# Kernel tuning notes

Measured on AMD Instinct MI355X. Metric: run time of the kernel, lower is better.

## Reference

```python
import jax, jax.numpy as jnp
import numpy as np

IN_DIM = 1024
OUT_DIM = 1024
NUM_HEADS = 16
DEPTH = IN_DIM // NUM_HEADS  # 64


def setup_inputs() -> dict:
    key = jax.random.key(0)
    ks = jax.random.split(key, 11)
    B, S = 8, 1024  # S must equal IN_DIM (reshape constraint in original module)
    s_in = 1.0 / np.sqrt(IN_DIM)
    return {
        "query": jax.random.normal(ks[0], (B, S, IN_DIM), jnp.float32),
        "key": jax.random.normal(ks[1], (B, S, IN_DIM), jnp.float32),
        "value": jax.random.normal(ks[2], (B, S, IN_DIM), jnp.float32),
        "Wq": jax.random.normal(ks[3], (IN_DIM, IN_DIM), jnp.float32) * s_in,
        "bq": jnp.zeros((IN_DIM,), jnp.float32),
        "Wk": jax.random.normal(ks[4], (IN_DIM, IN_DIM), jnp.float32) * s_in,
        "bk": jnp.zeros((IN_DIM,), jnp.float32),
        "Wv": jax.random.normal(ks[5], (IN_DIM, IN_DIM), jnp.float32) * s_in,
        "bv": jnp.zeros((IN_DIM,), jnp.float32),
        "Wo": jax.random.normal(ks[6], (OUT_DIM, IN_DIM), jnp.float32) * s_in,
        "bo": jnp.zeros((OUT_DIM,), jnp.float32),
    }


def reference(query, key, value, Wq, bq, Wk, bk, Wv, bv, Wo, bo):
    B, S, D = query.shape
    H, P = NUM_HEADS, DEPTH

    def split_heads(x):
        # (B,S,D) -> (B,S,H,P) -> transpose last two dims -> (B,S,P,H)
        return x.reshape(B, S, H, P).swapaxes(-1, -2)

    Q = split_heads(query @ Wq.T + bq)   # (B,S,P,H)
    K = split_heads(key @ Wk.T + bk)     # (B,S,P,H)
    V = split_heads(value @ Wv.T + bv)   # (B,S,P,H)

    scale = jnp.sqrt(jnp.float32(P))
    # scores over the depth axis, per (batch, token): (B,S,P,P)
    scores = jnp.einsum('bsph,bsqh->bspq', Q, K) / scale
    # original uses softmax over dim=0 (the batch axis) - reproduce faithfully
    attn = jax.nn.softmax(scores, axis=0)
    out = jnp.einsum('bspq,bsqh->bsph', attn, V)   # (B,S,P,H)
    # transpose(-1,-2) -> (B,S,H,P), reshape to (B,S,S) (requires H*P == S)
    out = out.swapaxes(-1, -2).reshape(B, S, S)
    out = out @ Wo.T + bo                           # (B,S,OUT_DIM)
    return jax.nn.sigmoid(out)
```

## Files before the change

### kernel.cpp

```cpp
#include <hip/hip_runtime.h>


using short8  = __attribute__((ext_vector_type(8))) short;
using floatx4 = __attribute__((ext_vector_type(4))) float;

__device__ __forceinline__ float bf2f(unsigned short u) {
    return __uint_as_float(((unsigned)u) << 16);
}
__device__ __forceinline__ unsigned short f2bf(float f) {
    unsigned u = __float_as_uint(f);
    u += 0x7fffu + ((u >> 16) & 1u);
    return (unsigned short)(u >> 16);
}
__device__ __forceinline__ unsigned pack_trunc(float f0, float f1) {
    return __builtin_amdgcn_perm(__float_as_uint(f1), __float_as_uint(f0), 0x07060302u);
}
__device__ __forceinline__ void async_ld16(const void* g, void* l) {
    __builtin_amdgcn_global_load_lds(
        (const __attribute__((address_space(1))) unsigned int*)g,
        (__attribute__((address_space(3))) unsigned int*)l, 16, 0, 0);
}

__device__ __forceinline__ void conv8(const float* src, unsigned short* d, size_t i) {
    float4 a = *(const float4*)(src + i);
    float4 b = *(const float4*)(src + i + 4);
    uint4 o;
    o.x = ((unsigned)f2bf(a.y) << 16) | f2bf(a.x);
    o.y = ((unsigned)f2bf(a.w) << 16) | f2bf(a.z);
    o.z = ((unsigned)f2bf(b.y) << 16) | f2bf(b.x);
    o.w = ((unsigned)f2bf(b.w) << 16) | f2bf(b.z);
    *(uint4*)(d + i) = o;
}

__global__ __launch_bounds__(256) void convert_weights(
    const float* __restrict__ w0, const float* __restrict__ w1,
    const float* __restrict__ w2, const float* __restrict__ w3,
    unsigned short* __restrict__ dst)
{
    const float* srcs[4] = {w0, w1, w2, w3};
    conv8(srcs[blockIdx.y], dst + (size_t)blockIdx.y * (1024u * 1024u),
          ((size_t)blockIdx.x * 256 + threadIdx.x) * 8);
}

__global__ __launch_bounds__(256) void convert_acts(
    const float* __restrict__ a0, const float* __restrict__ a1,
    const float* __restrict__ a2, unsigned short* __restrict__ dst)
{
    const float* srcs[3] = {a0, a1, a2};
    conv8(srcs[blockIdx.y], dst + (size_t)blockIdx.y * ((size_t)8192 * 1024),
          ((size_t)blockIdx.x * 256 + threadIdx.x) * 8);
}

template<bool AF32, bool SIG>
__global__ __launch_bounds__(256) void gemm128(
    const void* __restrict__ A0, const void* __restrict__ A1, const void* __restrict__ A2,
    const unsigned short* __restrict__ W0, const unsigned short* __restrict__ W1,
    const unsigned short* __restrict__ W2,
    const float* __restrict__ b0, const float* __restrict__ b1, const float* __restrict__ b2,
    void* __restrict__ C0, void* __restrict__ C1, void* __restrict__ C2)
{
    const int z = blockIdx.z;
    const void* Ap = (z == 0) ? A0 : (z == 1) ? A1 : A2;
    const unsigned short* W = (z == 0) ? W0 : (z == 1) ? W1 : W2;
    const float* bias = (z == 0) ? b0 : (z == 1) ? b1 : b2;
    void* Cp = (z == 0) ? C0 : (z == 1) ? C1 : C2;

    constexpr int Kd = 1024, Nd = 1024;
    const int t = threadIdx.x;
    const int w = t >> 6, lane = t & 63;
    const int l15 = lane & 15, quad = lane >> 4;
    const int blockM = blockIdx.x * 128;
    const int blockN = blockIdx.y * 128;
    const int wy = w >> 1, wx = w & 1;

    __shared__ unsigned short Bs[128 * 32];
    constexpr int ABYTES = AF32 ? (128 * 32 * 4) : (128 * 32 * 2);
    __shared__ __align__(16) unsigned char AsRaw[ABYTES];
    float* AsF = (float*)AsRaw;
    unsigned short* AsB = (unsigned short*)AsRaw;

    const int br  = lane >> 2;
    const int bg  = (lane & 3) ^ (br & 3);
    const unsigned short* Bsrc0 = W + (size_t)(blockN + w * 32 + br) * Kd + bg * 8;
    const unsigned short* Bsrc1 = Bsrc0 + (size_t)16 * Kd;
    unsigned short* Bdst0 = &Bs[(w * 2 + 0) * 512];
    unsigned short* Bdst1 = &Bs[(w * 2 + 1) * 512];

    const int ar = lane >> 3;
    const int ag = (lane & 7) ^ (ar & 7);
    const float* AsrcF[4];
    float* AdstF[4];
    const unsigned short* AsrcB0 = nullptr; const unsigned short* AsrcB1 = nullptr;
    unsigned short* AdstB0 = nullptr; unsigned short* AdstB1 = nullptr;
    if (AF32) {
        #pragma unroll
        for (int j = 0; j < 4; ++j) {
            AsrcF[j] = (const float*)Ap + (size_t)(blockM + w * 32 + j * 8 + ar) * Kd + ag * 4;
            AdstF[j] = AsF + (w * 4 + j) * 256;
        }
    } else {
        AsrcB0 = (const unsigned short*)Ap + (size_t)(blockM + w * 32 + br) * Kd + bg * 8;
        AsrcB1 = AsrcB0 + (size_t)16 * Kd;
        AdstB0 = &AsB[(w * 2 + 0) * 512];
        AdstB1 = &AsB[(w * 2 + 1) * 512];
    }

    floatx4 acc[4][4] = {};

    for (int k0 = 0; k0 < Kd; k0 += 32) {
        if (AF32) {
            #pragma unroll
            for (int j = 0; j < 4; ++j) async_ld16(AsrcF[j] + k0, AdstF[j]);
        } else {
            async_ld16(AsrcB0 + k0, AdstB0);
            async_ld16(AsrcB1 + k0, AdstB1);
        }
        async_ld16(Bsrc0 + k0, Bdst0);
        async_ld16(Bsrc1 + k0, Bdst1);
        __syncthreads();

        short8 af[4], bfr[4];
        #pragma unroll
        for (int mt = 0; mt < 4; ++mt) {
            const int row = wy * 64 + mt * 16 + l15;
            if (AF32) {
                const int r7 = l15 & 7;
                const float* ap = AsF + row * 32;
                float4 lo = *(const float4*)(ap + (((quad * 2 + 0) ^ r7) * 4));
                float4 hi = *(const float4*)(ap + (((quad * 2 + 1) ^ r7) * 4));
                union { unsigned u[4]; short8 s; } cv;
                cv.u[0] = pack_trunc(lo.x, lo.y);
                cv.u[1] = pack_trunc(lo.z, lo.w);
                cv.u[2] = pack_trunc(hi.x, hi.y);
                cv.u[3] = pack_trunc(hi.z, hi.w);
                af[mt] = cv.s;
            } else {
                af[mt] = *(const short8*)&AsB[row * 32 + (quad ^ (l15 & 3)) * 8];
            }
        }
        #pragma unroll
        for (int nt = 0; nt < 4; ++nt) {
            const int row = wx * 64 + nt * 16 + l15;
            bfr[nt] = *(const short8*)&Bs[row * 32 + (quad ^ (l15 & 3)) * 8];
        }
        #pragma unroll
        for (int mt = 0; mt < 4; ++mt)
            #pragma unroll
            for (int nt = 0; nt < 4; ++nt)
                acc[mt][nt] = __builtin_amdgcn_mfma_f32_16x16x32_bf16(af[mt], bfr[nt], acc[mt][nt], 0, 0, 0);
        __syncthreads();
    }

    #pragma unroll
    for (int nt = 0; nt < 4; ++nt) {
        const int col = blockN + wx * 64 + nt * 16 + l15;
        const float bv = bias[col];
        #pragma unroll
        for (int mt = 0; mt < 4; ++mt) {
            const int row = blockM + wy * 64 + mt * 16 + quad * 4;
            #pragma unroll
            for (int r = 0; r < 4; ++r) {
                float v = acc[mt][nt][r] + bv;
                if (SIG) {
                    v = 1.0f / (1.0f + __expf(-v));
                    ((float*)Cp)[(size_t)(row + r) * Nd + col] = v;
                } else {
                    ((unsigned short*)Cp)[(size_t)(row + r) * Nd + col] = f2bf(v);
                }
            }
        }
    }
}

__device__ __forceinline__ float dot4q(const float* qf, ushort4 k) {
    return qf[0] * bf2f(k.x) + qf[1] * bf2f(k.y) + qf[2] * bf2f(k.z) + qf[3] * bf2f(k.w);
}
__device__ __forceinline__ void axpy4(float* o, float w, ushort4 v) {
    o[0] += w * bf2f(v.x); o[1] += w * bf2f(v.y); o[2] += w * bf2f(v.z); o[3] += w * bf2f(v.w);
}

__global__ __launch_bounds__(512) void attn_kernel(
    const unsigned short* __restrict__ Q,
    const unsigned short* __restrict__ Kt,
    const unsigned short* __restrict__ Vt,
    unsigned short* __restrict__ O2)
{
    constexpr int QS = 20;
    constexpr int PB = 64 * QS + 4;
    __shared__ unsigned short Kl[8 * PB];
    __shared__ unsigned short Vl[8 * PB];
    __shared__ unsigned short Ql[8 * PB];

    const int s = blockIdx.x;
    const int t = threadIdx.x;
    const int b8 = t >> 6, lq = t & 63;

    {
        const size_t gbase = ((size_t)b8 * 1024 + s) * 1024;
        const unsigned short* Ks = Kt + gbase;
        const unsigned short* Vs = Vt + gbase;
        const unsigned short* Qs = Q  + gbase;
        unsigned* kd = (unsigned*)&Kl[b8 * PB + lq * QS];
        unsigned* vd = (unsigned*)&Vl[b8 * PB + lq * QS];
        unsigned* qd = (unsigned*)&Ql[b8 * PB + lq * QS];
        #pragma unroll
        for (int w2 = 0; w2 < 8; ++w2) {
            unsigned klo = Ks[(2 * w2) * 64 + lq], khi = Ks[(2 * w2 + 1) * 64 + lq];
            kd[w2] = klo | (khi << 16);
            unsigned vlo = Vs[(2 * w2) * 64 + lq], vhi = Vs[(2 * w2 + 1) * 64 + lq];
            vd[w2] = vlo | (vhi << 16);
            unsigned qlo = Qs[(2 * w2) * 64 + lq], qhi = Qs[(2 * w2 + 1) * 64 + lq];
            qd[w2] = qlo | (qhi << 16);
        }
    }
    __syncthreads();

    const int b = t & 7;
    const int p = t >> 3;

    float qf[16], o[16];
    {
        const unsigned short* qp = &Ql[b * PB + p * QS];
        #pragma unroll
        for (int h4 = 0; h4 < 4; ++h4) {
            ushort4 qv = *(const ushort4*)&qp[h4 * 4];
            qf[h4 * 4 + 0] = bf2f(qv.x); qf[h4 * 4 + 1] = bf2f(qv.y);
            qf[h4 * 4 + 2] = bf2f(qv.z); qf[h4 * 4 + 3] = bf2f(qv.w);
        }
        #pragma unroll
        for (int h = 0; h < 16; ++h) o[h] = 0.0f;
    }

    const unsigned short* kp = &Kl[b * PB];
    const unsigned short* vp = &Vl[b * PB];

    for (int q = 0; q < 64; ++q) {
        const int off = q * QS;
        float sc = dot4q(qf + 0,  *(const ushort4*)&kp[off + 0])
                 + dot4q(qf + 4,  *(const ushort4*)&kp[off + 4])
                 + dot4q(qf + 8,  *(const ushort4*)&kp[off + 8])
                 + dot4q(qf + 12, *(const ushort4*)&kp[off + 12]);
        float e = __expf(sc * 0.125f);
        float d = e;
        d += __shfl_xor(d, 1);
        d += __shfl_xor(d, 2);
        d += __shfl_xor(d, 4);
        const float wgt = e * __builtin_amdgcn_rcpf(d);
        axpy4(o + 0,  wgt, *(const ushort4*)&vp[off + 0]);
        axpy4(o + 4,  wgt, *(const ushort4*)&vp[off + 4]);
        axpy4(o + 8,  wgt, *(const ushort4*)&vp[off + 8]);
        axpy4(o + 12, wgt, *(const ushort4*)&vp[off + 12]);
    }

    {
        unsigned* od = (unsigned*)&Ql[b * PB + p * QS];
        #pragma unroll
        for (int w2 = 0; w2 < 8; ++w2)
            od[w2] = ((unsigned)f2bf(o[2 * w2 + 1]) << 16) | f2bf(o[2 * w2]);
    }
    __syncthreads();

    {
        const size_t gbase = ((size_t)b8 * 1024 + s) * 1024;
        const unsigned* qd = (const unsigned*)&Ql[b8 * PB + lq * QS];
        #pragma unroll
        for (int w2 = 0; w2 < 8; ++w2) {
            unsigned v = qd[w2];
            O2[gbase + (2 * w2) * 64 + lq]     = (unsigned short)(v & 0xffff);
            O2[gbase + (2 * w2 + 1) * 64 + lq] = (unsigned short)(v >> 16);
        }
    }
}

extern "C" void kernel_launch(void* const* d_in, const int* in_sizes, int n_in,
                              void* d_out, int out_size, void* d_ws, size_t ws_size,
                              hipStream_t stream) {
    const float* query = (const float*)d_in[0];
    const float* key_  = (const float*)d_in[1];
    const float* value = (const float*)d_in[2];
    const float* Wq = (const float*)d_in[3];
    const float* bq = (const float*)d_in[4];
    const float* Wk = (const float*)d_in[5];
    const float* bk = (const float*)d_in[6];
    const float* Wv = (const float*)d_in[7];
    const float* bv = (const float*)d_in[8];
    const float* Wo = (const float*)d_in[9];
    const float* bo = (const float*)d_in[10];

    const size_t WN = (size_t)1024 * 1024;
    const size_t MN = (size_t)8192 * 1024;

    unsigned short* Wbf = (unsigned short*)d_ws;
    unsigned short* Wq_bf = Wbf;
    unsigned short* Wk_bf = Wbf + WN;
    unsigned short* Wv_bf = Wbf + 2 * WN;
    unsigned short* Wo_bf = Wbf + 3 * WN;

    convert_weights<<<dim3(512, 4), dim3(256), 0, stream>>>(Wq, Wk, Wv, Wo, Wbf);

    const bool big = ws_size >= (4 * WN + 6 * MN) * sizeof(unsigned short);

    unsigned short* Qb; unsigned short* Kb; unsigned short* Vb;
    if (big) {
        unsigned short* abf = Wbf + 4 * WN;
        Qb = abf + 3 * MN; Kb = Qb + MN; Vb = Kb + MN;
        convert_acts<<<dim3(4096, 3), dim3(256), 0, stream>>>(query, key_, value, abf);
        gemm128<false, false><<<dim3(64, 8, 3), dim3(256), 0, stream>>>(
            abf, abf + MN, abf + 2 * MN, Wq_bf, Wk_bf, Wv_bf, bq, bk, bv, Qb, Kb, Vb);
    } else {
        Qb = Wbf + 4 * WN; Kb = Qb + MN; Vb = Kb + MN;
        gemm128<true, false><<<dim3(64, 8, 3), dim3(256), 0, stream>>>(
            query, key_, value, Wq_bf, Wk_bf, Wv_bf, bq, bk, bv, Qb, Kb, Vb);
    }

    unsigned short* O2 = Qb;
    attn_kernel<<<dim3(1024), dim3(512), 0, stream>>>(Qb, Kb, Vb, O2);

    gemm128<false, true><<<dim3(64, 8, 1), dim3(256), 0, stream>>>(
        O2, O2, O2, Wo_bf, Wo_bf, Wo_bf, bo, bo, bo, d_out, d_out, d_out);
}
```

Baseline: 329.0 us.

## Rewrite batch-axis attention with MFMA score and PV products

Replaces the scalar per-thread dot-product attention kernel with one that computes QK^T and attn·V through bf16 MFMA instructions. The batch-axis softmax is done as a separate pass over exp scores staged in LDS. The grid is split in two along the query-row dimension, so each block handles 32 rows of P. This trades scalar FMA work for matrix-core throughput, at the cost of extra LDS staging and syncs, bf16 truncation of the exp values, and K/V being loaded twice across the two halves. Because O2 aliases Q, correctness depends on each half writing only its own 32-row slice.

```diff
diff --git a/kernel.cpp b/kernel.cpp
--- a/kernel.cpp
+++ b/kernel.cpp
@@ -1,8 +1,9 @@
 #include <hip/hip_runtime.h>
 
 
-using short8  = __attribute__((ext_vector_type(8))) short;
-using floatx4 = __attribute__((ext_vector_type(4))) float;
+using short8   = __attribute__((ext_vector_type(8))) short;
+using floatx4  = __attribute__((ext_vector_type(4))) float;
+using floatx16 = __attribute__((ext_vector_type(16))) float;
 
 __device__ __forceinline__ float bf2f(unsigned short u) {
     return __uint_as_float(((unsigned)u) << 16);
@@ -172,102 +173,140 @@
     }
 }
 
-__device__ __forceinline__ float dot4q(const float* qf, ushort4 k) {
-    return qf[0] * bf2f(k.x) + qf[1] * bf2f(k.y) + qf[2] * bf2f(k.z) + qf[3] * bf2f(k.w);
-}
-__device__ __forceinline__ void axpy4(float* o, float w, ushort4 v) {
-    o[0] += w * bf2f(v.x); o[1] += w * bf2f(v.y); o[2] += w * bf2f(v.z); o[3] += w * bf2f(v.w);
-}
-
-__global__ __launch_bounds__(512) void attn_kernel(
+__global__ __launch_bounds__(512) void attn_mfma(
     const unsigned short* __restrict__ Q,
     const unsigned short* __restrict__ Kt,
     const unsigned short* __restrict__ Vt,
     unsigned short* __restrict__ O2)
 {
-    constexpr int QS = 20;
-    constexpr int PB = 64 * QS + 4;
-    __shared__ unsigned short Kl[8 * PB];
-    __shared__ unsigned short Vl[8 * PB];
-    __shared__ unsigned short Ql[8 * PB];
-
-    const int s = blockIdx.x;
-    const int t = threadIdx.x;
-    const int b8 = t >> 6, lq = t & 63;
-
-    {
-        const size_t gbase = ((size_t)b8 * 1024 + s) * 1024;
-        const unsigned short* Ks = Kt + gbase;
-        const unsigned short* Vs = Vt + gbase;
-        const unsigned short* Qs = Q  + gbase;
-        unsigned* kd = (unsigned*)&Kl[b8 * PB + lq * QS];
-        unsigned* vd = (unsigned*)&Vl[b8 * PB + lq * QS];
-        unsigned* qd = (unsigned*)&Ql[b8 * PB + lq * QS];
-        #pragma unroll
-        for (int w2 = 0; w2 < 8; ++w2) {
-            unsigned klo = Ks[(2 * w2) * 64 + lq], khi = Ks[(2 * w2 + 1) * 64 + lq];
-            kd[w2] = klo | (khi << 16);
-            unsigned vlo = Vs[(2 * w2) * 64 + lq], vhi = Vs[(2 * w2 + 1) * 64 + lq];
-            vd[w2] = vlo | (vhi << 16);
-            unsigned qlo = Qs[(2 * w2) * 64 + lq], qhi = Qs[(2 * w2 + 1) * 64 + lq];
-            qd[w2] = qlo | (qhi << 16);
-        }
-    }
-    __syncthreads();
-
-    const int b = t & 7;
-    const int p = t >> 3;
-
-    float qf[16], o[16];
-    {
-        const unsigned short* qp = &Ql[b * PB + p * QS];
-        #pragma unroll
-        for (int h4 = 0; h4 < 4; ++h4) {
-            ushort4 qv = *(const ushort4*)&qp[h4 * 4];
-            qf[h4 * 4 + 0] = bf2f(qv.x); qf[h4 * 4 + 1] = bf2f(qv.y);
-            qf[h4 * 4 + 2] = bf2f(qv.z); qf[h4 * 4 + 3] = bf2f(qv.w);
-        }
-        #pragma unroll
-        for (int h = 0; h < 16; ++h) o[h] = 0.0f;
-    }
-
-    const unsigned short* kp = &Kl[b * PB];
-    const unsigned short* vp = &Vl[b * PB];
-
-    for (int q = 0; q < 64; ++q) {
-        const int off = q * QS;
-        float sc = dot4q(qf + 0,  *(const ushort4*)&kp[off + 0])
-                 + dot4q(qf + 4,  *(const ushort4*)&kp[off + 4])
-                 + dot4q(qf + 8,  *(const ushort4*)&kp[off + 8])
-                 + dot4q(qf + 12, *(const ushort4*)&kp[off + 12]);
-        float e = __expf(sc * 0.125f);
-        float d = e;
-        d += __shfl_xor(d, 1);
-        d += __shfl_xor(d, 2);
-        d += __shfl_xor(d, 4);
-        const float wgt = e * __builtin_amdgcn_rcpf(d);
-        axpy4(o + 0,  wgt, *(const ushort4*)&vp[off + 0]);
-        axpy4(o + 4,  wgt, *(const ushort4*)&vp[off + 4]);
-        axpy4(o + 8,  wgt, *(const ushort4*)&vp[off + 8]);
-        axpy4(o + 12, wgt, *(const ushort4*)&vp[off + 12]);
-    }
-
-    {
-        unsigned* od = (unsigned*)&Ql[b * PB + p * QS];
-        #pragma unroll
-        for (int w2 = 0; w2 < 8; ++w2)
-            od[w2] = ((unsigned)f2bf(o[2 * w2 + 1]) << 16) | f2bf(o[2 * w2]);
-    }
-    __syncthreads();
-
-    {
-        const size_t gbase = ((size_t)b8 * 1024 + s) * 1024;
-        const unsigned* qd = (const unsigned*)&Ql[b8 * PB + lq * QS];
-        #pragma unroll
-        for (int w2 = 0; w2 < 8; ++w2) {
-            unsigned v = qd[w2];
-            O2[gbase + (2 * w2) * 64 + lq]     = (unsigned short)(v & 0xffff);
-            O2[gbase + (2 * w2 + 1) * 64 + lq] = (unsigned short)(v >> 16);
+    constexpr int VOFF = 0;
+    constexpr int UOFF = 9216;
+    constexpr int QOFF = UOFF + 8192;
+    __shared__ __align__(16) unsigned short lds[UOFF + 18432];
+
+    const int s  = blockIdx.x;
+    const int ph = blockIdx.y;
+    const int t  = threadIdx.x;
+    const int w  = t >> 6;
+    const int l  = t & 63;
+    const int l15 = l & 15, l31 = l & 31, half = l >> 5, quad = l >> 4;
+
+    const size_t gb = ((size_t)w * 1024 + s) * 1024;
+
+    {
+        const unsigned* vg = (const unsigned*)(Vt + gb);
+        unsigned* vd = (unsigned*)lds;
+        #pragma unroll
+        for (int it = 0; it < 8; ++it) {
+            const int h = it * 2 + half;
+            vd[w * 576 + h * 36 + l31] = vg[h * 32 + l31];
+        }
+        const unsigned short* kg = Kt + gb;
+        unsigned* kd = (unsigned*)(lds + UOFF);
+        #pragma unroll
+        for (int h2 = 0; h2 < 8; ++h2) {
+            unsigned klo = kg[(2 * h2) * 64 + l];
+            unsigned khi = kg[(2 * h2 + 1) * 64 + l];
+            kd[w * 512 + l * 8 + h2] = klo | (khi << 16);
+        }
+        const unsigned short* qg = Q + gb + ph * 32;
+        unsigned* qd = (unsigned*)(lds + QOFF);
+        #pragma unroll
+        for (int it = 0; it < 4; ++it) {
+            const int h = it * 4 + half * 2;
+            unsigned qlo = qg[h * 64 + l31];
+            unsigned qhi = qg[(h + 1) * 64 + l31];
+            qd[w * 256 + l31 * 8 + it * 2 + half] = qlo | (qhi << 16);
+        }
+    }
+    __syncthreads();
+
+    floatx16 sc[2];
+    {
+        short8 qf = *(const short8*)&lds[QOFF + w * 512 + l31 * 16 + half * 8];
+        short8 kf0 = *(const short8*)&lds[UOFF + w * 1024 + l31 * 16 + half * 8];
+        short8 kf1 = *(const short8*)&lds[UOFF + w * 1024 + (32 + l31) * 16 + half * 8];
+        floatx16 z = {};
+        sc[0] = __builtin_amdgcn_mfma_f32_32x32x16_bf16(kf0, qf, z, 0, 0, 0);
+        sc[1] = __builtin_amdgcn_mfma_f32_32x32x16_bf16(kf1, qf, z, 0, 0, 0);
+    }
+    __syncthreads();
+
+    {
+        unsigned short* sx = lds + UOFF + w * 2304 + l31 * 72;
+        #pragma unroll
+        for (int nt = 0; nt < 2; ++nt) {
+            #pragma unroll
+            for (int rg = 0; rg < 4; ++rg) {
+                float e0 = __expf(sc[nt][4 * rg + 0] * 0.125f);
+                float e1 = __expf(sc[nt][4 * rg + 1] * 0.125f);
+                float e2 = __expf(sc[nt][4 * rg + 2] * 0.125f);
+                float e3 = __expf(sc[nt][4 * rg + 3] * 0.125f);
+                uint2 pk = { pack_trunc(e0, e1), pack_trunc(e2, e3) };
+                const int q0 = nt * 32 + rg * 8 + half * 4;
+                *(uint2*)&sx[q0] = pk;
+            }
+        }
+    }
+    __syncthreads();
+
+    {
+        const int p  = t & 31;
+        const int q0 = (t >> 5) * 4;
+        unsigned short* base = lds + UOFF + p * 72 + q0;
+        float fv[8][4];
+        float den0 = 0.f, den1 = 0.f, den2 = 0.f, den3 = 0.f;
+        #pragma unroll
+        for (int b = 0; b < 8; ++b) {
+            uint2 v = *(const uint2*)&base[b * 2304];
+            fv[b][0] = bf2f((unsigned short)(v.x & 0xffff));
+            fv[b][1] = bf2f((unsigned short)(v.x >> 16));
+            fv[b][2] = bf2f((unsigned short)(v.y & 0xffff));
+            fv[b][3] = bf2f((unsigned short)(v.y >> 16));
+            den0 += fv[b][0]; den1 += fv[b][1]; den2 += fv[b][2]; den3 += fv[b][3];
+        }
+        const float r0 = __builtin_amdgcn_rcpf(den0);
+        const float r1 = __builtin_amdgcn_rcpf(den1);
+        const float r2 = __builtin_amdgcn_rcpf(den2);
+        const float r3 = __builtin_amdgcn_rcpf(den3);
+        #pragma unroll
+        for (int b = 0; b < 8; ++b) {
+            uint2 pk = { pack_trunc(fv[b][0] * r0, fv[b][1] * r1),
+                         pack_trunc(fv[b][2] * r2, fv[b][3] * r3) };
+            *(uint2*)&base[b * 2304] = pk;
+        }
+    }
+    __syncthreads();
+
+    floatx4 o[2] = {};
+    #pragma unroll
+    for (int qc = 0; qc < 2; ++qc) {
+        short8 vf = *(const short8*)&lds[VOFF + w * 1152 + l15 * 72 + qc * 32 + quad * 8];
+        #pragma unroll
+        for (int mt = 0; mt < 2; ++mt) {
+            short8 wf = *(const short8*)&lds[UOFF + w * 2304 + (mt * 16 + l15) * 72 + qc * 32 + quad * 8];
+            o[mt] = __builtin_amdgcn_mfma_f32_16x16x32_bf16(wf, vf, o[mt], 0, 0, 0);
+        }
+    }
+    {
+        unsigned short* ol = lds + UOFF + w * 2304 + l15 * 36;
+        #pragma unroll
+        for (int mt = 0; mt < 2; ++mt) {
+            uint2 pk = { pack_trunc(o[mt][0], o[mt][1]), pack_trunc(o[mt][2], o[mt][3]) };
+            *(uint2*)&ol[mt * 16 + quad * 4] = pk;
+        }
+    }
+    __syncthreads();
+
+    {
+        unsigned* outdw = (unsigned*)O2;
+        const unsigned* ol = (const unsigned*)(lds + UOFF + w * 2304);
+        const size_t gdw = ((size_t)w * 1024 + s) * 512 + ph * 16;
+        #pragma unroll
+        for (int i = 0; i < 4; ++i) {
+            const int d = i * 64 + l;
+            const int h = d >> 4, pq = d & 15;
+            outdw[gdw + h * 32 + pq] = ol[h * 18 + pq];
         }
     }
 }
@@ -314,7 +353,7 @@
     }
 
     unsigned short* O2 = Qb;
-    attn_kernel<<<dim3(1024), dim3(512), 0, stream>>>(Qb, Kb, Vb, O2);
+    attn_mfma<<<dim3(1024, 2), dim3(512), 0, stream>>>(Qb, Kb, Vb, O2);
 
     gemm128<false, true><<<dim3(64, 8, 1), dim3(256), 0, stream>>>(
         O2, O2, O2, Wo_bf, Wo_bf, Wo_bf, bo, bo, bo, d_out, d_out, d_out);
```

Result: faster. 282.3 us (-14.2%).
